# Performance work log

Measured on AMD Instinct MI355X. Metric: run time of the kernel, lower is better.

## Reference

```python
import jax, jax.numpy as jnp
import numpy as np

WINDOW = 7
DIM = 128
HEADS = 4
HEAD_DIM = DIM // HEADS
SCALE = HEAD_DIM ** -0.5
BW = 4096  # number of windows
N = WINDOW * WINDOW  # 49 tokens per window


def _relative_position_index(ws: int) -> np.ndarray:
    coords = np.stack(np.meshgrid(np.arange(ws), np.arange(ws), indexing='ij'))  # [2,ws,ws]
    cf = coords.reshape(2, -1)  # [2, n]
    rel = cf[:, :, None] - cf[:, None, :]  # [2, n, n]
    rel = rel.transpose(1, 2, 0).copy()
    rel[:, :, 0] += ws - 1
    rel[:, :, 1] += ws - 1
    rel[:, :, 0] *= 2 * ws - 1
    return rel.sum(-1)  # [n, n] int


def setup_inputs() -> dict:
    key = jax.random.key(0)
    ks = jax.random.split(key, 6)
    table_size = (2 * WINDOW - 1) ** 2  # 169
    x = jax.random.normal(ks[0], (BW, N, DIM), dtype=jnp.float32)
    qkv_w = jax.random.normal(ks[1], (3 * DIM, DIM), dtype=jnp.float32) * (DIM ** -0.5)
    qkv_b = jnp.zeros((3 * DIM,), dtype=jnp.float32)
    proj_w = jax.random.normal(ks[2], (DIM, DIM), dtype=jnp.float32) * (DIM ** -0.5)
    proj_b = jnp.zeros((DIM,), dtype=jnp.float32)
    bias_table = jax.random.normal(ks[3], (table_size, HEADS), dtype=jnp.float32) * 0.02
    rel_index = jnp.asarray(_relative_position_index(WINDOW), dtype=jnp.int32)  # [n, n]
    return {"x": x, "qkv_w": qkv_w, "qkv_b": qkv_b, "proj_w": proj_w,
            "proj_b": proj_b, "bias_table": bias_table, "rel_index": rel_index}


def reference(x, qkv_w, qkv_b, proj_w, proj_b, bias_table, rel_index):
    b, n, c = x.shape
    # fused qkv projection: [b, n, 3*dim]
    qkv = x @ qkv_w.T + qkv_b
    qkv = qkv.reshape(b, n, 3, HEADS, HEAD_DIM).transpose(2, 0, 3, 1, 4)  # [3,b,h,n,hd]
    q, k, v = qkv[0], qkv[1], qkv[2]
    # windowed attention logits: [b, h, n, n]
    attn = jnp.einsum('bhqd,bhkd->bhqk', q * SCALE, k)
    # relative position bias gather: table[rel_index] -> [n, n, h] -> [h, n, n]
    bias = bias_table[rel_index].transpose(2, 0, 1)
    attn = jax.nn.softmax(attn + bias[None], axis=-1)
    out = jnp.einsum('bhqk,bhkd->bhqd', attn, v)
    out = out.transpose(0, 2, 1, 3).reshape(b, n, c)
    return out @ proj_w.T + proj_b
```

## Files before the change

### kernel.cpp

```cpp
#include <hip/hip_runtime.h>

#define NWIN 4096
#define NTOK 49
#define DIMC 128
#define QK_SCALE 0.17677669529663689f
#define LOG2E 1.4426950408889634f

typedef __attribute__((ext_vector_type(8))) short vs8;
typedef __attribute__((ext_vector_type(4))) float vf4;
typedef __attribute__((ext_vector_type(2))) unsigned vu2;
typedef __attribute__((ext_vector_type(4))) _Float16 vh4;
typedef __attribute__((ext_vector_type(8))) _Float16 vh8;
typedef __attribute__((ext_vector_type(2))) __fp16 vp2;

#define NO_CSE() asm volatile("" ::: "memory")
#define SWZ(row) (((row) & 15) << 4)

__device__ __forceinline__ unsigned cvtpk(float a, float b) {
  unsigned r;
  asm("v_cvt_pk_bf16_f32 %0, %1, %2" : "=v"(r) : "v"(a), "v"(b));
  return r;
}

__device__ __forceinline__ float exp2f_raw(float x) {
  float r;
  asm("v_exp_f32 %0, %1" : "=v"(r) : "v"(x));
  return r;
}

__device__ __forceinline__ vh4 pack4h(float a0, float a1, float a2, float a3) {
  union { vh4 v; vp2 h[2]; } u;
  u.h[0] = __builtin_amdgcn_cvt_pkrtz(a0, a1);
  u.h[1] = __builtin_amdgcn_cvt_pkrtz(a2, a3);
  return u.v;
}

__device__ __forceinline__ vh8 cat8(vh4 a, vh4 b) {
  union { vh8 v8; vh4 v4[2]; } u;
  u.v4[0] = a; u.v4[1] = b;
  return u.v8;
}

__device__ __forceinline__ vf4 unpack_bf4(vu2 b) {
  union { unsigned u; float f; } a0, a1, a2, a3;
  a0.u = b[0] << 16; a1.u = b[0] & 0xffff0000u;
  a2.u = b[1] << 16; a3.u = b[1] & 0xffff0000u;
  return (vf4){a0.f, a1.f, a2.f, a3.f};
}

__device__ __forceinline__ short f2bf(float f) {
  union { float f; unsigned u; } x; x.f = f;
  unsigned r = x.u + 0x7fffu + ((x.u >> 16) & 1u);
  return (short)(r >> 16);
}

__global__ void prep_kernel(const float* __restrict__ qkv_w, const float* __restrict__ proj_w,
                            const float* __restrict__ bias_table, const int* __restrict__ rel_index,
                            short* __restrict__ qkv_wb, short* __restrict__ proj_wb,
                            short* __restrict__ bias_bf) {
  int i = blockIdx.x * 256 + threadIdx.x;
  if (i < 49152) qkv_wb[i] = f2bf(qkv_w[i]);
  int j = i - 49152;
  if (j >= 0 && j < 16384) proj_wb[j] = f2bf(proj_w[j]);
  int k = i - 65536;
  if (k >= 0 && k < 16384) {
    int h = k >> 12, rc = k & 4095, r = rc >> 6, c = rc & 63;
    float v = -1e30f;
    if (r < NTOK && c < NTOK) v = bias_table[rel_index[r * NTOK + c] * 4 + h];
    bias_bf[k] = f2bf(v * LOG2E);
  }
}

__launch_bounds__(256)
__global__ void win_attn(const float* __restrict__ x,
                         const float* __restrict__ qkv_b,
                         const float* __restrict__ proj_b,
                         const short* __restrict__ qkv_wb,
                         const short* __restrict__ proj_wb,
                         const short* __restrict__ bias_bf,
                         float* __restrict__ out) {
  __shared__ __align__(16) char lds[32768];
  char* const ldsA = lds;
  char* const ldsB = lds + 16384;

  const int tid  = threadIdx.x;
  const int lane = tid & 63;
  const int w    = tid >> 6;
  const int l15  = lane & 15;
  const int g    = lane >> 4;
  const int winA = blockIdx.x * 2;

  const float* xwA = x + (size_t)winA * (NTOK * DIMC);
  const float* xwB = xwA + NTOK * DIMC;
  vf4 aA[4], bA[4], aB[4], bB[4];
  int srow[4], sc16[4];
#pragma unroll
  for (int it = 0; it < 4; ++it) {
    int chunk = tid + it * 256;
    srow[it] = chunk >> 4; sc16[it] = chunk & 15;
    if (srow[it] < NTOK) {
      const float* sA = xwA + srow[it] * DIMC + sc16[it] * 8;
      const float* sB = xwB + srow[it] * DIMC + sc16[it] * 8;
      aA[it] = *(const vf4*)sA; bA[it] = *(const vf4*)(sA + 4);
      aB[it] = *(const vf4*)sB; bB[it] = *(const vf4*)(sB + 4);
    }
  }

  vs8 bwQ[4], bwK[4];
  vf4 qbQ, qbK;
  {
    const short* wrQ = qkv_wb + ((2 * w) * 16 + l15) * DIMC;
    const short* wrK = qkv_wb + ((8 + 2 * w) * 16 + l15) * DIMC;
#pragma unroll
    for (int kk = 0; kk < 4; ++kk) {
      bwQ[kk] = *(const vs8*)(wrQ + kk * 32 + g * 8);
      bwK[kk] = *(const vs8*)(wrK + kk * 32 + g * 8);
    }
    qbQ = *(const vf4*)(qkv_b + (2 * w) * 16 + g * 4);
    qbK = *(const vf4*)(qkv_b + (8 + 2 * w) * 16 + g * 4);
  }

#pragma unroll
  for (int it = 0; it < 4; ++it) {
    union { vs8 s; unsigned u[4]; } pA, pB;
    if (srow[it] < NTOK) {
      pA.u[0] = cvtpk(aA[it].x, aA[it].y); pA.u[1] = cvtpk(aA[it].z, aA[it].w);
      pA.u[2] = cvtpk(bA[it].x, bA[it].y); pA.u[3] = cvtpk(bA[it].z, bA[it].w);
      pB.u[0] = cvtpk(aB[it].x, aB[it].y); pB.u[1] = cvtpk(aB[it].z, aB[it].w);
      pB.u[2] = cvtpk(bB[it].x, bB[it].y); pB.u[3] = cvtpk(bB[it].z, bB[it].w);
    } else {
      pA.u[0] = pA.u[1] = pA.u[2] = pA.u[3] = 0u;
      pB.u[0] = pB.u[1] = pB.u[2] = pB.u[3] = 0u;
    }
    int off = srow[it] * 256 + ((sc16[it] * 16) ^ SWZ(srow[it]));
    *(vs8*)(ldsA + off) = pA.s;
    *(vs8*)(ldsB + off) = pB.s;
  }
  __syncthreads();

  vh4 qB[2][4], qBB[2][4], kA[2][4], kAB[2][4], vA[2][4], vAB[2][4];
  const float QSC2 = QK_SCALE * LOG2E;
  vs8 bwV[4];
  float bvV;
#pragma unroll
  for (int dt = 0; dt < 2; ++dt) {
    {
      const int cV = 16 + 2 * w + dt;
      const short* wr = qkv_wb + (cV * 16 + l15) * DIMC;
#pragma unroll
      for (int kk = 0; kk < 4; ++kk) bwV[kk] = *(const vs8*)(wr + kk * 32 + g * 8);
      bvV = qkv_b[cV * 16 + l15];
    }
    NO_CSE();
    {
      vf4 aQ[2][4], aK[2][4];
#pragma unroll
      for (int tr = 0; tr < 4; ++tr) {
        aQ[0][tr] = qbQ; aQ[1][tr] = qbQ;
        aK[0][tr] = qbK; aK[1][tr] = qbK;
      }
      __builtin_amdgcn_s_setprio(1);
#pragma unroll
      for (int kk = 0; kk < 4; ++kk)
#pragma unroll
        for (int tr = 0; tr < 4; ++tr) {
          int row = tr * 16 + l15;
          int off = row * 256 + ((kk * 64 + g * 16) ^ SWZ(row));
          vs8 fA = *(const vs8*)(ldsA + off);
          vs8 fB = *(const vs8*)(ldsB + off);
          aQ[0][tr] = __builtin_amdgcn_mfma_f32_16x16x32_bf16(bwQ[kk], fA, aQ[0][tr], 0, 0, 0);
          aK[0][tr] = __builtin_amdgcn_mfma_f32_16x16x32_bf16(bwK[kk], fA, aK[0][tr], 0, 0, 0);
          aQ[1][tr] = __builtin_amdgcn_mfma_f32_16x16x32_bf16(bwQ[kk], fB, aQ[1][tr], 0, 0, 0);
          aK[1][tr] = __builtin_amdgcn_mfma_f32_16x16x32_bf16(bwK[kk], fB, aK[1][tr], 0, 0, 0);
        }
      __builtin_amdgcn_s_setprio(0);
#pragma unroll
      for (int tr = 0; tr < 4; ++tr) {
        qB[dt][tr]  = pack4h(aQ[0][tr][0] * QSC2, aQ[0][tr][1] * QSC2, aQ[0][tr][2] * QSC2, aQ[0][tr][3] * QSC2);
        qBB[dt][tr] = pack4h(aQ[1][tr][0] * QSC2, aQ[1][tr][1] * QSC2, aQ[1][tr][2] * QSC2, aQ[1][tr][3] * QSC2);
        kA[dt][tr]  = pack4h(aK[0][tr][0], aK[0][tr][1], aK[0][tr][2], aK[0][tr][3]);
        kAB[dt][tr] = pack4h(aK[1][tr][0], aK[1][tr][1], aK[1][tr][2], aK[1][tr][3]);
      }
    }
    if (dt == 0) {
      const short* wrQ = qkv_wb + ((2 * w + 1) * 16 + l15) * DIMC;
      const short* wrK = qkv_wb + ((8 + 2 * w + 1) * 16 + l15) * DIMC;
#pragma unroll
      for (int kk = 0; kk < 4; ++kk) {
        bwQ[kk] = *(const vs8*)(wrQ + kk * 32 + g * 8);
        bwK[kk] = *(const vs8*)(wrK + kk * 32 + g * 8);
      }
      qbQ = *(const vf4*)(qkv_b + (2 * w + 1) * 16 + g * 4);
      qbK = *(const vf4*)(qkv_b + (8 + 2 * w + 1) * 16 + g * 4);
    }
    NO_CSE();
    {
      vf4 aV[2][4];
#pragma unroll
      for (int tr = 0; tr < 4; ++tr) {
        aV[0][tr] = (vf4){bvV, bvV, bvV, bvV};
        aV[1][tr] = aV[0][tr];
      }
      __builtin_amdgcn_s_setprio(1);
#pragma unroll
      for (int kk = 0; kk < 4; ++kk)
#pragma unroll
        for (int tr = 0; tr < 4; ++tr) {
          int row = tr * 16 + l15;
          int off = row * 256 + ((kk * 64 + g * 16) ^ SWZ(row));
          vs8 fA = *(const vs8*)(ldsA + off);
          vs8 fB = *(const vs8*)(ldsB + off);
          aV[0][tr] = __builtin_amdgcn_mfma_f32_16x16x32_bf16(fA, bwV[kk], aV[0][tr], 0, 0, 0);
          aV[1][tr] = __builtin_amdgcn_mfma_f32_16x16x32_bf16(fB, bwV[kk], aV[1][tr], 0, 0, 0);
        }
      __builtin_amdgcn_s_setprio(0);
#pragma unroll
      for (int tr = 0; tr < 4; ++tr) {
        vA[dt][tr]  = pack4h(aV[0][tr][0], aV[0][tr][1], aV[0][tr][2], aV[0][tr][3]);
        vAB[dt][tr] = pack4h(aV[1][tr][0], aV[1][tr][1], aV[1][tr][2], aV[1][tr][3]);
      }
    }
  }

  const short* bpb = bias_bf + w * 4096;
  vu2 cinC[4];
#pragma unroll
  for (int tcK = 0; tcK < 4; ++tcK)
    cinC[tcK] = *(const vu2*)(bpb + l15 * 64 + tcK * 16 + g * 4);
  __syncthreads();

#pragma unroll
  for (int trQ = 0; trQ < 4; ++trQ) {
    const int q = trQ * 16 + l15;
    vu2 cinN[4];
    if (trQ < 3) {
#pragma unroll
      for (int tcK = 0; tcK < 4; ++tcK)
        cinN[tcK] = *(const vu2*)(bpb + (q + 16) * 64 + tcK * 16 + g * 4);
    }
    const vh8 q8A = cat8(qB[0][trQ], qB[1][trQ]);
    const vh8 q8B = cat8(qBB[0][trQ], qBB[1][trQ]);
    vf4 sA[4], sB[4];
    __builtin_amdgcn_s_setprio(1);
#pragma unroll
    for (int tcK = 0; tcK < 4; ++tcK) {
      vf4 cin = unpack_bf4(cinC[tcK]);
      sA[tcK] = __builtin_amdgcn_mfma_f32_16x16x32_f16(cat8(kA[0][tcK], kA[1][tcK]), q8A, cin, 0, 0, 0);
      sB[tcK] = __builtin_amdgcn_mfma_f32_16x16x32_f16(cat8(kAB[0][tcK], kAB[1][tcK]), q8B, cin, 0, 0, 0);
    }
    __builtin_amdgcn_s_setprio(0);
    float sumA = 0.f, sumB = 0.f;
#pragma unroll
    for (int tcK = 0; tcK < 4; ++tcK)
#pragma unroll
      for (int r = 0; r < 4; ++r) {
        float eA = exp2f_raw(sA[tcK][r]); sA[tcK][r] = eA; sumA += eA;
        float eB = exp2f_raw(sB[tcK][r]); sB[tcK][r] = eB; sumB += eB;
      }
    sumA += __shfl_xor(sumA, 16, 64);
    sumB += __shfl_xor(sumB, 16, 64);
    sumA += __shfl_xor(sumA, 32, 64);
    sumB += __shfl_xor(sumB, 32, 64);
    float ivA = 1.0f / sumA, ivB = 1.0f / sumB;
    vh4 pA[4], pB[4];
#pragma unroll
    for (int tcK = 0; tcK < 4; ++tcK) {
      pA[tcK] = pack4h(sA[tcK][0], sA[tcK][1], sA[tcK][2], sA[tcK][3]);
      pB[tcK] = pack4h(sB[tcK][0], sB[tcK][1], sB[tcK][2], sB[tcK][3]);
    }
    vf4 o0A = (vf4){0.f,0.f,0.f,0.f}, o1A = o0A, o0B = o0A, o1B = o0A;
    __builtin_amdgcn_s_setprio(1);
#pragma unroll
    for (int tp = 0; tp < 2; ++tp) {
      const vh8 p8A = cat8(pA[2 * tp], pA[2 * tp + 1]);
      const vh8 p8B = cat8(pB[2 * tp], pB[2 * tp + 1]);
      o0A = __builtin_amdgcn_mfma_f32_16x16x32_f16(cat8(vA[0][2 * tp], vA[0][2 * tp + 1]), p8A, o0A, 0, 0, 0);
      o0B = __builtin_amdgcn_mfma_f32_16x16x32_f16(cat8(vAB[0][2 * tp], vAB[0][2 * tp + 1]), p8B, o0B, 0, 0, 0);
      o1A = __builtin_amdgcn_mfma_f32_16x16x32_f16(cat8(vA[1][2 * tp], vA[1][2 * tp + 1]), p8A, o1A, 0, 0, 0);
      o1B = __builtin_amdgcn_mfma_f32_16x16x32_f16(cat8(vAB[1][2 * tp], vAB[1][2 * tp + 1]), p8B, o1B, 0, 0, 0);
    }
    __builtin_amdgcn_s_setprio(0);
    {
      int db0 = (w * 32 + g * 4) * 2;
      int db1 = (w * 32 + 16 + g * 4) * 2;
      int o0 = q * 256 + (db0 ^ SWZ(q));
      int o1 = q * 256 + (db1 ^ SWZ(q));
      vu2 p;
      p[0] = cvtpk(o0A[0] * ivA, o0A[1] * ivA); p[1] = cvtpk(o0A[2] * ivA, o0A[3] * ivA);
      *(vu2*)(ldsA + o0) = p;
      p[0] = cvtpk(o1A[0] * ivA, o1A[1] * ivA); p[1] = cvtpk(o1A[2] * ivA, o1A[3] * ivA);
      *(vu2*)(ldsA + o1) = p;
      p[0] = cvtpk(o0B[0] * ivB, o0B[1] * ivB); p[1] = cvtpk(o0B[2] * ivB, o0B[3] * ivB);
      *(vu2*)(ldsB + o0) = p;
      p[0] = cvtpk(o1B[0] * ivB, o1B[1] * ivB); p[1] = cvtpk(o1B[2] * ivB, o1B[3] * ivB);
      *(vu2*)(ldsB + o1) = p;
    }
#pragma unroll
    for (int tcK = 0; tcK < 4; ++tcK) cinC[tcK] = cinN[tcK];
  }

  vs8 bw2[2][4];
  vf4 pb2[2];
#pragma unroll
  for (int ci = 0; ci < 2; ++ci) {
    int ct = w + ci * 4;
    const short* wr = proj_wb + (ct * 16 + l15) * DIMC;
#pragma unroll
    for (int kk = 0; kk < 4; ++kk) bw2[ci][kk] = *(const vs8*)(wr + kk * 32 + g * 8);
    pb2[ci] = *(const vf4*)(proj_b + ct * 16 + g * 4);
  }
  __syncthreads();

  float* outA = out + (size_t)winA * (NTOK * DIMC);
  float* outB = outA + NTOK * DIMC;
  {
    NO_CSE();
    vf4 acc[2][2][4];
#pragma unroll
    for (int ci = 0; ci < 2; ++ci)
#pragma unroll
      for (int tr = 0; tr < 4; ++tr) { acc[ci][0][tr] = pb2[ci]; acc[ci][1][tr] = pb2[ci]; }
    __builtin_amdgcn_s_setprio(1);
#pragma unroll
    for (int kk = 0; kk < 4; ++kk)
#pragma unroll
      for (int tr = 0; tr < 4; ++tr) {
        int row = tr * 16 + l15;
        int off = row * 256 + ((kk * 64 + g * 16) ^ SWZ(row));
        vs8 fA = *(const vs8*)(ldsA + off);
        vs8 fB = *(const vs8*)(ldsB + off);
        acc[0][0][tr] = __builtin_amdgcn_mfma_f32_16x16x32_bf16(bw2[0][kk], fA, acc[0][0][tr], 0, 0, 0);
        acc[1][0][tr] = __builtin_amdgcn_mfma_f32_16x16x32_bf16(bw2[1][kk], fA, acc[1][0][tr], 0, 0, 0);
        acc[0][1][tr] = __builtin_amdgcn_mfma_f32_16x16x32_bf16(bw2[0][kk], fB, acc[0][1][tr], 0, 0, 0);
        acc[1][1][tr] = __builtin_amdgcn_mfma_f32_16x16x32_bf16(bw2[1][kk], fB, acc[1][1][tr], 0, 0, 0);
      }
    __builtin_amdgcn_s_setprio(0);
#pragma unroll
    for (int ci = 0; ci < 2; ++ci) {
      int ct = w + ci * 4;
#pragma unroll
      for (int tr = 0; tr < 4; ++tr) {
        int token = tr * 16 + l15;
        if (token < NTOK) {
          *(vf4*)(outA + token * DIMC + ct * 16 + g * 4) = acc[ci][0][tr];
          *(vf4*)(outB + token * DIMC + ct * 16 + g * 4) = acc[ci][1][tr];
        }
      }
    }
  }
}

extern "C" void kernel_launch(void* const* d_in, const int* in_sizes, int n_in,
                              void* d_out, int out_size, void* d_ws, size_t ws_size,
                              hipStream_t stream) {
  const float* x          = (const float*)d_in[0];
  const float* qkv_w      = (const float*)d_in[1];
  const float* qkv_b      = (const float*)d_in[2];
  const float* proj_w     = (const float*)d_in[3];
  const float* proj_b     = (const float*)d_in[4];
  const float* bias_table = (const float*)d_in[5];
  const int*   rel_index  = (const int*)d_in[6];
  float* out = (float*)d_out;

  short* qkv_wb   = (short*)d_ws;
  short* proj_wb  = (short*)((char*)d_ws + 98304);
  short* bias_bf  = (short*)((char*)d_ws + 131072);

  prep_kernel<<<320, 256, 0, stream>>>(qkv_w, proj_w, bias_table, rel_index,
                                       qkv_wb, proj_wb, bias_bf);
  win_attn<<<NWIN / 2, 256, 0, stream>>>(x, qkv_b, proj_b, qkv_wb, proj_wb, bias_bf, out);
}
```

Before: 77.37 us.

## Make attention kernel persistent with double-buffered LDS prefetch of next window pair

The launch shrinks to 512 blocks, and each block loops over four window pairs. While attention runs on the current pair, the next pair's x is loaded into registers, converted to bf16 and written into the other half of a 64KB double-buffered LDS. The goal is to hide global load latency and spread launch overhead across more work per block. In exchange the block uses more LDS and more registers, which may lower occupancy, and the pass count is fixed by the 4096-window size.

```diff
diff --git a/kernel.cpp b/kernel.cpp
--- a/kernel.cpp
+++ b/kernel.cpp
@@ -1,8 +1,9 @@
 #include <hip/hip_runtime.h>
 
 #define NWIN 4096
+#define DIMC 128
 #define NTOK 49
-#define DIMC 128
+#define NBLK 512
 #define QK_SCALE 0.17677669529663689f
 #define LOG2E 1.4426950408889634f
 
@@ -79,31 +80,22 @@
                          const short* __restrict__ proj_wb,
                          const short* __restrict__ bias_bf,
                          float* __restrict__ out) {
-  __shared__ __align__(16) char lds[32768];
-  char* const ldsA = lds;
-  char* const ldsB = lds + 16384;
+  __shared__ __align__(16) char lds[65536];
 
   const int tid  = threadIdx.x;
   const int lane = tid & 63;
   const int w    = tid >> 6;
   const int l15  = lane & 15;
   const int g    = lane >> 4;
-  const int winA = blockIdx.x * 2;
-
-  const float* xwA = x + (size_t)winA * (NTOK * DIMC);
-  const float* xwB = xwA + NTOK * DIMC;
-  vf4 aA[4], bA[4], aB[4], bB[4];
-  int srow[4], sc16[4];
+  const float QSC2 = QK_SCALE * LOG2E;
+  const short* bpb = bias_bf + w * 4096;
+
+  int srow[4], sc16[4], soff[4];
 #pragma unroll
   for (int it = 0; it < 4; ++it) {
     int chunk = tid + it * 256;
     srow[it] = chunk >> 4; sc16[it] = chunk & 15;
-    if (srow[it] < NTOK) {
-      const float* sA = xwA + srow[it] * DIMC + sc16[it] * 8;
-      const float* sB = xwB + srow[it] * DIMC + sc16[it] * 8;
-      aA[it] = *(const vf4*)sA; bA[it] = *(const vf4*)(sA + 4);
-      aB[it] = *(const vf4*)sB; bB[it] = *(const vf4*)(sB + 4);
-    }
+    soff[it] = srow[it] * 256 + ((sc16[it] * 16) ^ SWZ(srow[it]));
   }
 
   vs8 bwQ[4], bwK[4];
@@ -120,45 +112,252 @@
     qbK = *(const vf4*)(qkv_b + (8 + 2 * w) * 16 + g * 4);
   }
 
-#pragma unroll
+  {
+    const float* xwA = x + (size_t)(2 * blockIdx.x) * (NTOK * DIMC);
+    const float* xwB = xwA + NTOK * DIMC;
+#pragma unroll
+    for (int it = 0; it < 4; ++it) {
+      union { vs8 s; unsigned u[4]; } pA, pB;
+      if (srow[it] < NTOK) {
+        const float* sA = xwA + srow[it] * DIMC + sc16[it] * 8;
+        const float* sB = xwB + srow[it] * DIMC + sc16[it] * 8;
+        vf4 a0 = *(const vf4*)sA, b0 = *(const vf4*)(sA + 4);
+        vf4 a1 = *(const vf4*)sB, b1 = *(const vf4*)(sB + 4);
+        pA.u[0] = cvtpk(a0.x, a0.y); pA.u[1] = cvtpk(a0.z, a0.w);
+        pA.u[2] = cvtpk(b0.x, b0.y); pA.u[3] = cvtpk(b0.z, b0.w);
+        pB.u[0] = cvtpk(a1.x, a1.y); pB.u[1] = cvtpk(a1.z, a1.w);
+        pB.u[2] = cvtpk(b1.x, b1.y); pB.u[3] = cvtpk(b1.z, b1.w);
+      } else {
+        pA.u[0] = pA.u[1] = pA.u[2] = pA.u[3] = 0u;
+        pB.u[0] = pB.u[1] = pB.u[2] = pB.u[3] = 0u;
+      }
+      *(vs8*)(lds + soff[it]) = pA.s;
+      *(vs8*)(lds + 16384 + soff[it]) = pB.s;
+    }
+  }
+
   for (int it = 0; it < 4; ++it) {
-    union { vs8 s; unsigned u[4]; } pA, pB;
-    if (srow[it] < NTOK) {
-      pA.u[0] = cvtpk(aA[it].x, aA[it].y); pA.u[1] = cvtpk(aA[it].z, aA[it].w);
-      pA.u[2] = cvtpk(bA[it].x, bA[it].y); pA.u[3] = cvtpk(bA[it].z, bA[it].w);
-      pB.u[0] = cvtpk(aB[it].x, aB[it].y); pB.u[1] = cvtpk(aB[it].z, aB[it].w);
-      pB.u[2] = cvtpk(bB[it].x, bB[it].y); pB.u[3] = cvtpk(bB[it].z, bB[it].w);
-    } else {
-      pA.u[0] = pA.u[1] = pA.u[2] = pA.u[3] = 0u;
-      pB.u[0] = pB.u[1] = pB.u[2] = pB.u[3] = 0u;
-    }
-    int off = srow[it] * 256 + ((sc16[it] * 16) ^ SWZ(srow[it]));
-    *(vs8*)(ldsA + off) = pA.s;
-    *(vs8*)(ldsB + off) = pB.s;
-  }
-  __syncthreads();
-
-  vh4 qB[2][4], qBB[2][4], kA[2][4], kAB[2][4], vA[2][4], vAB[2][4];
-  const float QSC2 = QK_SCALE * LOG2E;
-  vs8 bwV[4];
-  float bvV;
-#pragma unroll
-  for (int dt = 0; dt < 2; ++dt) {
+    const int winA = 2 * (blockIdx.x + it * NBLK);
+    char* const ldsA = lds + ((it & 1) << 15);
+    char* const ldsB = ldsA + 16384;
+    char* const nxtA = lds + (((it + 1) & 1) << 15);
+    char* const nxtB = nxtA + 16384;
+    __syncthreads();
+
+    vh4 qB[2][4], qBB[2][4], kA[2][4], kAB[2][4], vA[2][4], vAB[2][4];
+    vs8 bwV[4];
+    float bvV;
+#pragma unroll
+    for (int dt = 0; dt < 2; ++dt) {
+      {
+        const int cV = 16 + 2 * w + dt;
+        const short* wr = qkv_wb + (cV * 16 + l15) * DIMC;
+#pragma unroll
+        for (int kk = 0; kk < 4; ++kk) bwV[kk] = *(const vs8*)(wr + kk * 32 + g * 8);
+        bvV = qkv_b[cV * 16 + l15];
+      }
+      NO_CSE();
+      {
+        vf4 aQ[2][4], aK[2][4];
+#pragma unroll
+        for (int tr = 0; tr < 4; ++tr) {
+          aQ[0][tr] = qbQ; aQ[1][tr] = qbQ;
+          aK[0][tr] = qbK; aK[1][tr] = qbK;
+        }
+        __builtin_amdgcn_s_setprio(1);
+#pragma unroll
+        for (int kk = 0; kk < 4; ++kk)
+#pragma unroll
+          for (int tr = 0; tr < 4; ++tr) {
+            int row = tr * 16 + l15;
+            int off = row * 256 + ((kk * 64 + g * 16) ^ SWZ(row));
+            vs8 fA = *(const vs8*)(ldsA + off);
+            vs8 fB = *(const vs8*)(ldsB + off);
+            aQ[0][tr] = __builtin_amdgcn_mfma_f32_16x16x32_bf16(bwQ[kk], fA, aQ[0][tr], 0, 0, 0);
+            aK[0][tr] = __builtin_amdgcn_mfma_f32_16x16x32_bf16(bwK[kk], fA, aK[0][tr], 0, 0, 0);
+            aQ[1][tr] = __builtin_amdgcn_mfma_f32_16x16x32_bf16(bwQ[kk], fB, aQ[1][tr], 0, 0, 0);
+            aK[1][tr] = __builtin_amdgcn_mfma_f32_16x16x32_bf16(bwK[kk], fB, aK[1][tr], 0, 0, 0);
+          }
+        __builtin_amdgcn_s_setprio(0);
+#pragma unroll
+        for (int tr = 0; tr < 4; ++tr) {
+          qB[dt][tr]  = pack4h(aQ[0][tr][0] * QSC2, aQ[0][tr][1] * QSC2, aQ[0][tr][2] * QSC2, aQ[0][tr][3] * QSC2);
+          qBB[dt][tr] = pack4h(aQ[1][tr][0] * QSC2, aQ[1][tr][1] * QSC2, aQ[1][tr][2] * QSC2, aQ[1][tr][3] * QSC2);
+          kA[dt][tr]  = pack4h(aK[0][tr][0], aK[0][tr][1], aK[0][tr][2], aK[0][tr][3]);
+          kAB[dt][tr] = pack4h(aK[1][tr][0], aK[1][tr][1], aK[1][tr][2], aK[1][tr][3]);
+        }
+      }
+      if (dt == 0) {
+        const short* wrQ = qkv_wb + ((2 * w + 1) * 16 + l15) * DIMC;
+        const short* wrK = qkv_wb + ((8 + 2 * w + 1) * 16 + l15) * DIMC;
+#pragma unroll
+        for (int kk = 0; kk < 4; ++kk) {
+          bwQ[kk] = *(const vs8*)(wrQ + kk * 32 + g * 8);
+          bwK[kk] = *(const vs8*)(wrK + kk * 32 + g * 8);
+        }
+        qbQ = *(const vf4*)(qkv_b + (2 * w + 1) * 16 + g * 4);
+        qbK = *(const vf4*)(qkv_b + (8 + 2 * w + 1) * 16 + g * 4);
+      }
+      NO_CSE();
+      {
+        vf4 aV[2][4];
+#pragma unroll
+        for (int tr = 0; tr < 4; ++tr) {
+          aV[0][tr] = (vf4){bvV, bvV, bvV, bvV};
+          aV[1][tr] = aV[0][tr];
+        }
+        __builtin_amdgcn_s_setprio(1);
+#pragma unroll
+        for (int kk = 0; kk < 4; ++kk)
+#pragma unroll
+          for (int tr = 0; tr < 4; ++tr) {
+            int row = tr * 16 + l15;
+            int off = row * 256 + ((kk * 64 + g * 16) ^ SWZ(row));
+            vs8 fA = *(const vs8*)(ldsA + off);
+            vs8 fB = *(const vs8*)(ldsB + off);
+            aV[0][tr] = __builtin_amdgcn_mfma_f32_16x16x32_bf16(fA, bwV[kk], aV[0][tr], 0, 0, 0);
+            aV[1][tr] = __builtin_amdgcn_mfma_f32_16x16x32_bf16(fB, bwV[kk], aV[1][tr], 0, 0, 0);
+          }
+        __builtin_amdgcn_s_setprio(0);
+#pragma unroll
+        for (int tr = 0; tr < 4; ++tr) {
+          vA[dt][tr]  = pack4h(aV[0][tr][0], aV[0][tr][1], aV[0][tr][2], aV[0][tr][3]);
+          vAB[dt][tr] = pack4h(aV[1][tr][0], aV[1][tr][1], aV[1][tr][2], aV[1][tr][3]);
+        }
+      }
+    }
+
+    vu2 cinC[4];
+#pragma unroll
+    for (int tcK = 0; tcK < 4; ++tcK)
+      cinC[tcK] = *(const vu2*)(bpb + l15 * 64 + tcK * 16 + g * 4);
+    __syncthreads();
+
+    vf4 naA[4], nbA[4], naB[4], nbB[4];
+    const bool more = (it < 3);
+    if (more) {
+      const float* xwA = x + (size_t)(2 * (blockIdx.x + (it + 1) * NBLK)) * (NTOK * DIMC);
+      const float* xwB = xwA + NTOK * DIMC;
+#pragma unroll
+      for (int k2 = 0; k2 < 4; ++k2) {
+        if (srow[k2] < NTOK) {
+          const float* sA = xwA + srow[k2] * DIMC + sc16[k2] * 8;
+          const float* sB = xwB + srow[k2] * DIMC + sc16[k2] * 8;
+          naA[k2] = *(const vf4*)sA; nbA[k2] = *(const vf4*)(sA + 4);
+          naB[k2] = *(const vf4*)sB; nbB[k2] = *(const vf4*)(sB + 4);
+        }
+      }
+    }
+
+#pragma unroll
+    for (int trQ = 0; trQ < 4; ++trQ) {
+      const int q = trQ * 16 + l15;
+      vu2 cinN[4];
+      if (trQ < 3) {
+#pragma unroll
+        for (int tcK = 0; tcK < 4; ++tcK)
+          cinN[tcK] = *(const vu2*)(bpb + (q + 16) * 64 + tcK * 16 + g * 4);
+      }
+      const vh8 q8A = cat8(qB[0][trQ], qB[1][trQ]);
+      const vh8 q8B = cat8(qBB[0][trQ], qBB[1][trQ]);
+      vf4 sA[4], sB[4];
+      __builtin_amdgcn_s_setprio(1);
+#pragma unroll
+      for (int tcK = 0; tcK < 4; ++tcK) {
+        vf4 cin = unpack_bf4(cinC[tcK]);
+        sA[tcK] = __builtin_amdgcn_mfma_f32_16x16x32_f16(cat8(kA[0][tcK], kA[1][tcK]), q8A, cin, 0, 0, 0);
+        sB[tcK] = __builtin_amdgcn_mfma_f32_16x16x32_f16(cat8(kAB[0][tcK], kAB[1][tcK]), q8B, cin, 0, 0, 0);
+      }
+      __builtin_amdgcn_s_setprio(0);
+      float sumA = 0.f, sumB = 0.f;
+#pragma unroll
+      for (int tcK = 0; tcK < 4; ++tcK)
+#pragma unroll
+        for (int r = 0; r < 4; ++r) {
+          float eA = exp2f_raw(sA[tcK][r]); sA[tcK][r] = eA; sumA += eA;
+          float eB = exp2f_raw(sB[tcK][r]); sB[tcK][r] = eB; sumB += eB;
+        }
+      sumA += __shfl_xor(sumA, 16, 64);
+      sumB += __shfl_xor(sumB, 16, 64);
+      sumA += __shfl_xor(sumA, 32, 64);
+      sumB += __shfl_xor(sumB, 32, 64);
+      float ivA = 1.0f / sumA, ivB = 1.0f / sumB;
+      vh4 pA[4], pB[4];
+#pragma unroll
+      for (int tcK = 0; tcK < 4; ++tcK) {
+        pA[tcK] = pack4h(sA[tcK][0], sA[tcK][1], sA[tcK][2], sA[tcK][3]);
+        pB[tcK] = pack4h(sB[tcK][0], sB[tcK][1], sB[tcK][2], sB[tcK][3]);
+      }
+      vf4 o0A = (vf4){0.f,0.f,0.f,0.f}, o1A = o0A, o0B = o0A, o1B = o0A;
+      __builtin_amdgcn_s_setprio(1);
+#pragma unroll
+      for (int tp = 0; tp < 2; ++tp) {
+        const vh8 p8A = cat8(pA[2 * tp], pA[2 * tp + 1]);
+        const vh8 p8B = cat8(pB[2 * tp], pB[2 * tp + 1]);
+        o0A = __builtin_amdgcn_mfma_f32_16x16x32_f16(cat8(vA[0][2 * tp], vA[0][2 * tp + 1]), p8A, o0A, 0, 0, 0);
+        o0B = __builtin_amdgcn_mfma_f32_16x16x32_f16(cat8(vAB[0][2 * tp], vAB[0][2 * tp + 1]), p8B, o0B, 0, 0, 0);
+        o1A = __builtin_amdgcn_mfma_f32_16x16x32_f16(cat8(vA[1][2 * tp], vA[1][2 * tp + 1]), p8A, o1A, 0, 0, 0);
+        o1B = __builtin_amdgcn_mfma_f32_16x16x32_f16(cat8(vAB[1][2 * tp], vAB[1][2 * tp + 1]), p8B, o1B, 0, 0, 0);
+      }
+      __builtin_amdgcn_s_setprio(0);
+      {
+        int db0 = (w * 32 + g * 4) * 2;
+        int db1 = (w * 32 + 16 + g * 4) * 2;
+        int o0 = q * 256 + (db0 ^ SWZ(q));
+        int o1 = q * 256 + (db1 ^ SWZ(q));
+        vu2 p;
+        p[0] = cvtpk(o0A[0] * ivA, o0A[1] * ivA); p[1] = cvtpk(o0A[2] * ivA, o0A[3] * ivA);
+        *(vu2*)(ldsA + o0) = p;
+        p[0] = cvtpk(o1A[0] * ivA, o1A[1] * ivA); p[1] = cvtpk(o1A[2] * ivA, o1A[3] * ivA);
+        *(vu2*)(ldsA + o1) = p;
+        p[0] = cvtpk(o0B[0] * ivB, o0B[1] * ivB); p[1] = cvtpk(o0B[2] * ivB, o0B[3] * ivB);
+        *(vu2*)(ldsB + o0) = p;
+        p[0] = cvtpk(o1B[0] * ivB, o1B[1] * ivB); p[1] = cvtpk(o1B[2] * ivB, o1B[3] * ivB);
+        *(vu2*)(ldsB + o1) = p;
+      }
+#pragma unroll
+      for (int tcK = 0; tcK < 4; ++tcK) cinC[tcK] = cinN[tcK];
+    }
+
+    if (more) {
+#pragma unroll
+      for (int k2 = 0; k2 < 4; ++k2) {
+        union { vs8 s; unsigned u[4]; } pA, pB;
+        if (srow[k2] < NTOK) {
+          pA.u[0] = cvtpk(naA[k2].x, naA[k2].y); pA.u[1] = cvtpk(naA[k2].z, naA[k2].w);
+          pA.u[2] = cvtpk(nbA[k2].x, nbA[k2].y); pA.u[3] = cvtpk(nbA[k2].z, nbA[k2].w);
+          pB.u[0] = cvtpk(naB[k2].x, naB[k2].y); pB.u[1] = cvtpk(naB[k2].z, naB[k2].w);
+          pB.u[2] = cvtpk(nbB[k2].x, nbB[k2].y); pB.u[3] = cvtpk(nbB[k2].z, nbB[k2].w);
+        } else {
+          pA.u[0] = pA.u[1] = pA.u[2] = pA.u[3] = 0u;
+          pB.u[0] = pB.u[1] = pB.u[2] = pB.u[3] = 0u;
+        }
+        *(vs8*)(nxtA + soff[k2]) = pA.s;
+        *(vs8*)(nxtB + soff[k2]) = pB.s;
+      }
+    }
+
+    vs8 bw2[2][4];
+    vf4 pb2[2];
+#pragma unroll
+    for (int ci = 0; ci < 2; ++ci) {
+      int ct = w + ci * 4;
+      const short* wr = proj_wb + (ct * 16 + l15) * DIMC;
+#pragma unroll
+      for (int kk = 0; kk < 4; ++kk) bw2[ci][kk] = *(const vs8*)(wr + kk * 32 + g * 8);
+      pb2[ci] = *(const vf4*)(proj_b + ct * 16 + g * 4);
+    }
+    __syncthreads();
+
+    float* outA = out + (size_t)winA * (NTOK * DIMC);
+    float* outB = outA + NTOK * DIMC;
     {
-      const int cV = 16 + 2 * w + dt;
-      const short* wr = qkv_wb + (cV * 16 + l15) * DIMC;
-#pragma unroll
-      for (int kk = 0; kk < 4; ++kk) bwV[kk] = *(const vs8*)(wr + kk * 32 + g * 8);
-      bvV = qkv_b[cV * 16 + l15];
-    }
-    NO_CSE();
-    {
-      vf4 aQ[2][4], aK[2][4];
-#pragma unroll
-      for (int tr = 0; tr < 4; ++tr) {
-        aQ[0][tr] = qbQ; aQ[1][tr] = qbQ;
-        aK[0][tr] = qbK; aK[1][tr] = qbK;
-      }
+      NO_CSE();
+      vf4 acc[2][2][4];
+#pragma unroll
+      for (int ci = 0; ci < 2; ++ci)
+#pragma unroll
+        for (int tr = 0; tr < 4; ++tr) { acc[ci][0][tr] = pb2[ci]; acc[ci][1][tr] = pb2[ci]; }
       __builtin_amdgcn_s_setprio(1);
 #pragma unroll
       for (int kk = 0; kk < 4; ++kk)
@@ -168,184 +367,36 @@
           int off = row * 256 + ((kk * 64 + g * 16) ^ SWZ(row));
           vs8 fA = *(const vs8*)(ldsA + off);
           vs8 fB = *(const vs8*)(ldsB + off);
-          aQ[0][tr] = __builtin_amdgcn_mfma_f32_16x16x32_bf16(bwQ[kk], fA, aQ[0][tr], 0, 0, 0);
-          aK[0][tr] = __builtin_amdgcn_mfma_f32_16x16x32_bf16(bwK[kk], fA, aK[0][tr], 0, 0, 0);
-          aQ[1][tr] = __builtin_amdgcn_mfma_f32_16x16x32_bf16(bwQ[kk], fB, aQ[1][tr], 0, 0, 0);
-          aK[1][tr] = __builtin_amdgcn_mfma_f32_16x16x32_bf16(bwK[kk], fB, aK[1][tr], 0, 0, 0);
+          acc[0][0][tr] = __builtin_amdgcn_mfma_f32_16x16x32_bf16(bw2[0][kk], fA, acc[0][0][tr], 0, 0, 0);
+          acc[1][0][tr] = __builtin_amdgcn_mfma_f32_16x16x32_bf16(bw2[1][kk], fA, acc[1][0][tr], 0, 0, 0);
+          acc[0][1][tr] = __builtin_amdgcn_mfma_f32_16x16x32_bf16(bw2[0][kk], fB, acc[0][1][tr], 0, 0, 0);
+          acc[1][1][tr] = __builtin_amdgcn_mfma_f32_16x16x32_bf16(bw2[1][kk], fB, acc[1][1][tr], 0, 0, 0);
         }
       __builtin_amdgcn_s_setprio(0);
 #pragma unroll
-      for (int tr = 0; tr < 4; ++tr) {
-        qB[dt][tr]  = pack4h(aQ[0][tr][0] * QSC2, aQ[0][tr][1] * QSC2, aQ[0][tr][2] * QSC2, aQ[0][tr][3] * QSC2);
-        qBB[dt][tr] = pack4h(aQ[1][tr][0] * QSC2, aQ[1][tr][1] * QSC2, aQ[1][tr][2] * QSC2, aQ[1][tr][3] * QSC2);
-        kA[dt][tr]  = pack4h(aK[0][tr][0], aK[0][tr][1], aK[0][tr][2], aK[0][tr][3]);
-        kAB[dt][tr] = pack4h(aK[1][tr][0], aK[1][tr][1], aK[1][tr][2], aK[1][tr][3]);
-      }
-    }
-    if (dt == 0) {
-      const short* wrQ = qkv_wb + ((2 * w + 1) * 16 + l15) * DIMC;
-      const short* wrK = qkv_wb + ((8 + 2 * w + 1) * 16 + l15) * DIMC;
+      for (int ci = 0; ci < 2; ++ci) {
+        int ct = w + ci * 4;
+#pragma unroll
+        for (int tr = 0; tr < 4; ++tr) {
+          int token = tr * 16 + l15;
+          if (token < NTOK) {
+            *(vf4*)(outA + token * DIMC + ct * 16 + g * 4) = acc[ci][0][tr];
+            *(vf4*)(outB + token * DIMC + ct * 16 + g * 4) = acc[ci][1][tr];
+          }
+        }
+      }
+    }
+
+    if (more) {
+      const short* wrQ = qkv_wb + ((2 * w) * 16 + l15) * DIMC;
+      const short* wrK = qkv_wb + ((8 + 2 * w) * 16 + l15) * DIMC;
 #pragma unroll
       for (int kk = 0; kk < 4; ++kk) {
         bwQ[kk] = *(const vs8*)(wrQ + kk * 32 + g * 8);
         bwK[kk] = *(const vs8*)(wrK + kk * 32 + g * 8);
       }
-      qbQ = *(const vf4*)(qkv_b + (2 * w + 1) * 16 + g * 4);
-      qbK = *(const vf4*)(qkv_b + (8 + 2 * w + 1) * 16 + g * 4);
-    }
-    NO_CSE();
-    {
-      vf4 aV[2][4];
-#pragma unroll
-      for (int tr = 0; tr < 4; ++tr) {
-        aV[0][tr] = (vf4){bvV, bvV, bvV, bvV};
-        aV[1][tr] = aV[0][tr];
-      }
-      __builtin_amdgcn_s_setprio(1);
-#pragma unroll
-      for (int kk = 0; kk < 4; ++kk)
-#pragma unroll
-        for (int tr = 0; tr < 4; ++tr) {
-          int row = tr * 16 + l15;
-          int off = row * 256 + ((kk * 64 + g * 16) ^ SWZ(row));
-          vs8 fA = *(const vs8*)(ldsA + off);
-          vs8 fB = *(const vs8*)(ldsB + off);
-          aV[0][tr] = __builtin_amdgcn_mfma_f32_16x16x32_bf16(fA, bwV[kk], aV[0][tr], 0, 0, 0);
-          aV[1][tr] = __builtin_amdgcn_mfma_f32_16x16x32_bf16(fB, bwV[kk], aV[1][tr], 0, 0, 0);
-        }
-      __builtin_amdgcn_s_setprio(0);
-#pragma unroll
-      for (int tr = 0; tr < 4; ++tr) {
-        vA[dt][tr]  = pack4h(aV[0][tr][0], aV[0][tr][1], aV[0][tr][2], aV[0][tr][3]);
-        vAB[dt][tr] = pack4h(aV[1][tr][0], aV[1][tr][1], aV[1][tr][2], aV[1][tr][3]);
-      }
-    }
-  }
-
-  const short* bpb = bias_bf + w * 4096;
-  vu2 cinC[4];
-#pragma unroll
-  for (int tcK = 0; tcK < 4; ++tcK)
-    cinC[tcK] = *(const vu2*)(bpb + l15 * 64 + tcK * 16 + g * 4);
-  __syncthreads();
-
-#pragma unroll
-  for (int trQ = 0; trQ < 4; ++trQ) {
-    const int q = trQ * 16 + l15;
-    vu2 cinN[4];
-    if (trQ < 3) {
-#pragma unroll
-      for (int tcK = 0; tcK < 4; ++tcK)
-        cinN[tcK] = *(const vu2*)(bpb + (q + 16) * 64 + tcK * 16 + g * 4);
-    }
-    const vh8 q8A = cat8(qB[0][trQ], qB[1][trQ]);
-    const vh8 q8B = cat8(qBB[0][trQ], qBB[1][trQ]);
-    vf4 sA[4], sB[4];
-    __builtin_amdgcn_s_setprio(1);
-#pragma unroll
-    for (int tcK = 0; tcK < 4; ++tcK) {
-      vf4 cin = unpack_bf4(cinC[tcK]);
-      sA[tcK] = __builtin_amdgcn_mfma_f32_16x16x32_f16(cat8(kA[0][tcK], kA[1][tcK]), q8A, cin, 0, 0, 0);
-      sB[tcK] = __builtin_amdgcn_mfma_f32_16x16x32_f16(cat8(kAB[0][tcK], kAB[1][tcK]), q8B, cin, 0, 0, 0);
-    }
-    __builtin_amdgcn_s_setprio(0);
-    float sumA = 0.f, sumB = 0.f;
-#pragma unroll
-    for (int tcK = 0; tcK < 4; ++tcK)
-#pragma unroll
-      for (int r = 0; r < 4; ++r) {
-        float eA = exp2f_raw(sA[tcK][r]); sA[tcK][r] = eA; sumA += eA;
-        float eB = exp2f_raw(sB[tcK][r]); sB[tcK][r] = eB; sumB += eB;
-      }
-    sumA += __shfl_xor(sumA, 16, 64);
-    sumB += __shfl_xor(sumB, 16, 64);
-    sumA += __shfl_xor(sumA, 32, 64);
-    sumB += __shfl_xor(sumB, 32, 64);
-    float ivA = 1.0f / sumA, ivB = 1.0f / sumB;
-    vh4 pA[4], pB[4];
-#pragma unroll
-    for (int tcK = 0; tcK < 4; ++tcK) {
-      pA[tcK] = pack4h(sA[tcK][0], sA[tcK][1], sA[tcK][2], sA[tcK][3]);
-      pB[tcK] = pack4h(sB[tcK][0], sB[tcK][1], sB[tcK][2], sB[tcK][3]);
-    }
-    vf4 o0A = (vf4){0.f,0.f,0.f,0.f}, o1A = o0A, o0B = o0A, o1B = o0A;
-    __builtin_amdgcn_s_setprio(1);
-#pragma unroll
-    for (int tp = 0; tp < 2; ++tp) {
-      const vh8 p8A = cat8(pA[2 * tp], pA[2 * tp + 1]);
-      const vh8 p8B = cat8(pB[2 * tp], pB[2 * tp + 1]);
-      o0A = __builtin_amdgcn_mfma_f32_16x16x32_f16(cat8(vA[0][2 * tp], vA[0][2 * tp + 1]), p8A, o0A, 0, 0, 0);
-      o0B = __builtin_amdgcn_mfma_f32_16x16x32_f16(cat8(vAB[0][2 * tp], vAB[0][2 * tp + 1]), p8B, o0B, 0, 0, 0);
-      o1A = __builtin_amdgcn_mfma_f32_16x16x32_f16(cat8(vA[1][2 * tp], vA[1][2 * tp + 1]), p8A, o1A, 0, 0, 0);
-      o1B = __builtin_amdgcn_mfma_f32_16x16x32_f16(cat8(vAB[1][2 * tp], vAB[1][2 * tp + 1]), p8B, o1B, 0, 0, 0);
-    }
-    __builtin_amdgcn_s_setprio(0);
-    {
-      int db0 = (w * 32 + g * 4) * 2;
-      int db1 = (w * 32 + 16 + g * 4) * 2;
-      int o0 = q * 256 + (db0 ^ SWZ(q));
-      int o1 = q * 256 + (db1 ^ SWZ(q));
-      vu2 p;
-      p[0] = cvtpk(o0A[0] * ivA, o0A[1] * ivA); p[1] = cvtpk(o0A[2] * ivA, o0A[3] * ivA);
-      *(vu2*)(ldsA + o0) = p;
-      p[0] = cvtpk(o1A[0] * ivA, o1A[1] * ivA); p[1] = cvtpk(o1A[2] * ivA, o1A[3] * ivA);
-      *(vu2*)(ldsA + o1) = p;
-      p[0] = cvtpk(o0B[0] * ivB, o0B[1] * ivB); p[1] = cvtpk(o0B[2] * ivB, o0B[3] * ivB);
-      *(vu2*)(ldsB + o0) = p;
-      p[0] = cvtpk(o1B[0] * ivB, o1B[1] * ivB); p[1] = cvtpk(o1B[2] * ivB, o1B[3] * ivB);
-      *(vu2*)(ldsB + o1) = p;
-    }
-#pragma unroll
-    for (int tcK = 0; tcK < 4; ++tcK) cinC[tcK] = cinN[tcK];
-  }
-
-  vs8 bw2[2][4];
-  vf4 pb2[2];
-#pragma unroll
-  for (int ci = 0; ci < 2; ++ci) {
-    int ct = w + ci * 4;
-    const short* wr = proj_wb + (ct * 16 + l15) * DIMC;
-#pragma unroll
-    for (int kk = 0; kk < 4; ++kk) bw2[ci][kk] = *(const vs8*)(wr + kk * 32 + g * 8);
-    pb2[ci] = *(const vf4*)(proj_b + ct * 16 + g * 4);
-  }
-  __syncthreads();
-
-  float* outA = out + (size_t)winA * (NTOK * DIMC);
-  float* outB = outA + NTOK * DIMC;
-  {
-    NO_CSE();
-    vf4 acc[2][2][4];
-#pragma unroll
-    for (int ci = 0; ci < 2; ++ci)
-#pragma unroll
-      for (int tr = 0; tr < 4; ++tr) { acc[ci][0][tr] = pb2[ci]; acc[ci][1][tr] = pb2[ci]; }
-    __builtin_amdgcn_s_setprio(1);
-#pragma unroll
-    for (int kk = 0; kk < 4; ++kk)
-#pragma unroll
-      for (int tr = 0; tr < 4; ++tr) {
-        int row = tr * 16 + l15;
-        int off = row * 256 + ((kk * 64 + g * 16) ^ SWZ(row));
-        vs8 fA = *(const vs8*)(ldsA + off);
-        vs8 fB = *(const vs8*)(ldsB + off);
-        acc[0][0][tr] = __builtin_amdgcn_mfma_f32_16x16x32_bf16(bw2[0][kk], fA, acc[0][0][tr], 0, 0, 0);
-        acc[1][0][tr] = __builtin_amdgcn_mfma_f32_16x16x32_bf16(bw2[1][kk], fA, acc[1][0][tr], 0, 0, 0);
-        acc[0][1][tr] = __builtin_amdgcn_mfma_f32_16x16x32_bf16(bw2[0][kk], fB, acc[0][1][tr], 0, 0, 0);
-        acc[1][1][tr] = __builtin_amdgcn_mfma_f32_16x16x32_bf16(bw2[1][kk], fB, acc[1][1][tr], 0, 0, 0);
-      }
-    __builtin_amdgcn_s_setprio(0);
-#pragma unroll
-    for (int ci = 0; ci < 2; ++ci) {
-      int ct = w + ci * 4;
-#pragma unroll
-      for (int tr = 0; tr < 4; ++tr) {
-        int token = tr * 16 + l15;
-        if (token < NTOK) {
-          *(vf4*)(outA + token * DIMC + ct * 16 + g * 4) = acc[ci][0][tr];
-          *(vf4*)(outB + token * DIMC + ct * 16 + g * 4) = acc[ci][1][tr];
-        }
-      }
+      qbQ = *(const vf4*)(qkv_b + (2 * w) * 16 + g * 4);
+      qbK = *(const vf4*)(qkv_b + (8 + 2 * w) * 16 + g * 4);
     }
   }
 }
@@ -368,5 +419,5 @@
 
   prep_kernel<<<320, 256, 0, stream>>>(qkv_w, proj_w, bias_table, rel_index,
                                        qkv_wb, proj_wb, bias_bf);
-  win_attn<<<NWIN / 2, 256, 0, stream>>>(x, qkv_b, proj_b, qkv_wb, proj_wb, bias_bf, out);
-}
+  win_attn<<<NBLK, 256, 0, stream>>>(x, qkv_b, proj_b, qkv_wb, proj_wb, bias_bf, out);
+}
```

Result: slower. 118.7 us (+53.4%).
